# Kernel optimization log

Measured on AMD Instinct MI355X. Metric: run time of the kernel, lower is better.

The kernel has to match this reference:

```python
import jax, jax.numpy as jnp
import numpy as np

NUM_EXPERTS = 4
TOPK = 1
TEMPERATURE = 1.0
NORM_TOPK_PROB = True
N_CLS = 1
N_REL = 4


def setup_inputs() -> dict:
    key = jax.random.key(0)
    ks = jax.random.split(key, 7)
    B, N_total, D, r, E = 64, 1029, 768, 64, NUM_EXPERTS
    x = jax.random.normal(ks[0], (B, N_total, D), dtype=jnp.float32)
    # parameters (torch Linear convention: weight [out, in])
    Wd = jax.random.normal(ks[1], (r, D), dtype=jnp.float32) * (1.0 / np.sqrt(D))
    Wg = jax.random.normal(ks[2], (E, r), dtype=jnp.float32) * (1.0 / np.sqrt(r))
    We = jax.random.normal(ks[3], (E, r, r), dtype=jnp.float32) * (1.0 / np.sqrt(r))
    be = jax.random.normal(ks[4], (E, r), dtype=jnp.float32) * 0.01
    Wu = jax.random.normal(ks[5], (D, r), dtype=jnp.float32) * (1.0 / np.sqrt(r))
    gamma = jnp.ones((D,), dtype=jnp.float32)  # LayerScale init_values=1.0
    return {"x": x, "Wd": Wd, "Wg": Wg, "We": We, "be": be, "Wu": Wu, "gamma": gamma}


def reference(x, Wd, Wg, We, be, Wu, gamma):
    # proj_down (bias=False) + exact GELU (nn.GELU default)
    h = jax.nn.gelu(jnp.einsum('bnd,rd->bnr', x, Wd), approximate=False)  # [B,Nt,r]
    cls_tok = h[:, :N_CLS, :]
    rel_tok = h[:, N_CLS:N_CLS + N_REL, :]
    t = h[:, N_CLS + N_REL:, :]                                           # [B,N,r]
    B, N, r = t.shape

    # gating: softmax scores, top-k selection
    logits = jnp.einsum('bnr,er->bne', t, Wg) / TEMPERATURE
    scores = jax.nn.softmax(logits, axis=-1)                              # [B,N,E]
    topk_w, topk_idx = jax.lax.top_k(scores, TOPK)                        # [B,N,K]
    if TOPK > 1 and NORM_TOPK_PROB:
        topk_w = topk_w / jnp.sum(topk_w, axis=-1, keepdims=True)

    # experts are tiny Linear(r,r): compute all experts densely, then gather.
    # Same math as per-expert gather/GEMM/scatter-combine in the source.
    expert_all = jnp.einsum('bnr,esr->bnes', t, We) + be                  # [B,N,E,r]
    idx_b = jnp.broadcast_to(topk_idx[..., None], (B, N, TOPK, r))
    sel = jnp.take_along_axis(expert_all, idx_b, axis=2)                  # [B,N,K,r]
    combine = jnp.sum(sel * topk_w[..., None], axis=2)                    # [B,N,r]

    full = jnp.concatenate([cls_tok, rel_tok, t + combine], axis=1)       # [B,Nt,r]
    # proj_up (bias=False) + LayerScale
    return jnp.einsum('bnr,dr->bnd', full, Wu) * gamma
```

## Files before the change

kernel.cpp:

```cpp
#include <hip/hip_runtime.h>
#include <math.h>


#define GELU(v) (0.5f*(v)*(1.0f + erff((v)*0.70710678118654752440f)))

typedef __attribute__((ext_vector_type(8))) short bf16x8;
typedef __attribute__((ext_vector_type(4))) float f32x4;

#define MFMA(a,b,c) __builtin_amdgcn_mfma_f32_16x16x32_bf16((a),(b),(c),0,0,0)

__device__ __forceinline__ unsigned pk_hi(float a, float b) {
  return (__float_as_uint(a) >> 16) | (__float_as_uint(b) & 0xFFFF0000u);
}
__device__ __forceinline__ float f_lo(float a) {
  return a - __uint_as_float(__float_as_uint(a) & 0xFFFF0000u);
}
union U8 { unsigned u[4]; bf16x8 v; uint4 q; };
__device__ __forceinline__ bf16x8 hi8(float4 f0, float4 f1) {
  U8 r; r.u[0]=pk_hi(f0.x,f0.y); r.u[1]=pk_hi(f0.z,f0.w);
        r.u[2]=pk_hi(f1.x,f1.y); r.u[3]=pk_hi(f1.z,f1.w); return r.v;
}
__device__ __forceinline__ bf16x8 lo8(float4 f0, float4 f1) {
  U8 r; r.u[0]=pk_hi(f_lo(f0.x),f_lo(f0.y)); r.u[1]=pk_hi(f_lo(f0.z),f_lo(f0.w));
        r.u[2]=pk_hi(f_lo(f1.x),f_lo(f1.y)); r.u[3]=pk_hi(f_lo(f1.z),f_lo(f1.w)); return r.v;
}

__global__ __launch_bounds__(256) void prep_pack(
    const float* __restrict__ Wd, const float* __restrict__ Wg,
    const float* __restrict__ We, const float* __restrict__ Wu,
    char* __restrict__ wp)
{
  int fid = blockIdx.x*4 + (threadIdx.x >> 6);
  if (fid >= 452) return;
  int lane = threadIdx.x & 63, lg = lane >> 4, lr = lane & 15;
  float v[8];
  int part;
  if (fid < 192) {
    part = fid & 1; int q = fid >> 1;
    int nt = q & 3; q >>= 2; int kc = q & 1, kt = q >> 1;
    int col = nt*16 + lr, k = kt*64 + kc*32 + lg*8;
    const float* p = Wd + (size_t)col*768 + k;
    #pragma unroll
    for (int e = 0; e < 8; ++e) v[e] = p[e];
  } else if (fid < 260) {
    int f = fid - 192; part = f & 1; int q = f >> 1;
    int nt = q % 17, kc = q / 17;
    int col = nt*16 + lr, k = kc*32 + lg*8;
    if (col < 256) {
      const float* p = We + (size_t)col*64 + k;
      #pragma unroll
      for (int e = 0; e < 8; ++e) v[e] = p[e];
    } else if (col < 260) {
      const float* p = Wg + (size_t)(col-256)*64 + k;
      #pragma unroll
      for (int e = 0; e < 8; ++e) v[e] = p[e];
    } else {
      #pragma unroll
      for (int e = 0; e < 8; ++e) v[e] = 0.f;
    }
  } else {
    int f = fid - 260; part = f & 1; int q = f >> 1;
    int kc = q & 1, nt = q >> 1;
    int col = nt*16 + lr, k = kc*32 + lg*8;
    const float* p = Wu + (size_t)col*64 + k;
    #pragma unroll
    for (int e = 0; e < 8; ++e) v[e] = p[e];
  }
  U8 r;
  if (part == 0) {
    r.u[0]=pk_hi(v[0],v[1]); r.u[1]=pk_hi(v[2],v[3]);
    r.u[2]=pk_hi(v[4],v[5]); r.u[3]=pk_hi(v[6],v[7]);
  } else {
    r.u[0]=pk_hi(f_lo(v[0]),f_lo(v[1])); r.u[1]=pk_hi(f_lo(v[2]),f_lo(v[3]));
    r.u[2]=pk_hi(f_lo(v[4]),f_lo(v[5])); r.u[3]=pk_hi(f_lo(v[6]),f_lo(v[7]));
  }
  *(uint4*)(wp + (size_t)fid*1024 + lane*16) = r.q;
}

__global__ __launch_bounds__(256) void fused(
    const float* __restrict__ x, const float* __restrict__ be,
    const float* __restrict__ gamma, const char* __restrict__ wp,
    float* __restrict__ out)
{
  __shared__ float sF[4][16][68];
  const int tid = threadIdx.x, bm = blockIdx.x;
  const int wv = tid >> 6, l = tid & 63, lg = l >> 4, lr = l & 15;
  const char* wpL = wp + l*16;

  const float* xrow = x + (size_t)(bm*64 + wv*16 + lr)*768;
  f32x4 t4[4];
  #pragma unroll
  for (int nt = 0; nt < 4; ++nt)
    #pragma unroll
    for (int r = 0; r < 4; ++r) t4[nt][r] = 0.f;

  for (int kt = 0; kt < 12; ++kt) {
    #pragma unroll
    for (int kc = 0; kc < 2; ++kc) {
      const float* xp = xrow + kt*64 + kc*32 + lg*8;
      float4 f0 = *(const float4*)xp, f1 = *(const float4*)(xp + 4);
      bf16x8 ah = hi8(f0, f1), al = lo8(f0, f1);
      const char* bp = wpL + (size_t)((kt*2 + kc)*8)*1024;
      #pragma unroll
      for (int nt = 0; nt < 4; ++nt) {
        bf16x8 bh = *(const bf16x8*)(bp + (nt*2+0)*1024);
        bf16x8 bl = *(const bf16x8*)(bp + (nt*2+1)*1024);
        t4[nt] = MFMA(ah, bh, t4[nt]);
        t4[nt] = MFMA(ah, bl, t4[nt]);
        t4[nt] = MFMA(al, bh, t4[nt]);
      }
    }
  }
  #pragma unroll
  for (int nt = 0; nt < 4; ++nt)
    #pragma unroll
    for (int r = 0; r < 4; ++r) {
      float g = GELU(t4[nt][r]);
      t4[nt][r] = g;
      sF[wv][lg*4 + r][nt*16 + lr] = g;
    }

  bf16x8 pah[2], pal[2];
  #pragma unroll
  for (int kc = 0; kc < 2; ++kc) {
    const float* ap = &sF[wv][lr][kc*32 + lg*8];
    float4 a0 = *(const float4*)ap, a1 = *(const float4*)(ap + 4);
    pah[kc] = hi8(a0, a1); pal[kc] = lo8(a0, a1);
  }
  f32x4 lac;
  #pragma unroll
  for (int r = 0; r < 4; ++r) lac[r] = 0.f;
  #pragma unroll
  for (int kc = 0; kc < 2; ++kc) {
    const char* bp = wpL + (size_t)(192 + (kc*17 + 16)*2)*1024;
    bf16x8 bh = *(const bf16x8*)(bp);
    bf16x8 bl = *(const bf16x8*)(bp + 1024);
    lac = MFMA(pah[kc], bh, lac);
    lac = MFMA(pah[kc], bl, lac);
    lac = MFMA(pal[kc], bh, lac);
  }
  const int tokbase = bm*64 + wv*16 + lg*4;
  float w_[4]; int ei_[4];
  #pragma unroll
  for (int r = 0; r < 4; ++r) {
    float lt = lac[r];
    int base = l & 48;
    float l0 = __shfl(lt, base+0), l1 = __shfl(lt, base+1);
    float l2 = __shfl(lt, base+2), l3 = __shfl(lt, base+3);
    int ei = 0; float lm = l0;
    if (l1 > lm) { lm = l1; ei = 1; }
    if (l2 > lm) { lm = l2; ei = 2; }
    if (l3 > lm) { lm = l3; ei = 3; }
    float s = expf(l0-lm) + expf(l1-lm) + expf(l2-lm) + expf(l3-lm);
    float w = 1.0f / s;
    int pos = (tokbase + r) % 1029;
    if (pos < 5) w = 0.0f;
    w_[r] = w; ei_[r] = ei;
  }
  f32x4 sel[4];
  #pragma unroll
  for (int j = 0; j < 4; ++j)
    #pragma unroll
    for (int r = 0; r < 4; ++r) sel[j][r] = 0.f;
  #pragma unroll
  for (int e = 0; e < 4; ++e) {
    f32x4 de[4];
    #pragma unroll
    for (int j = 0; j < 4; ++j)
      #pragma unroll
      for (int r = 0; r < 4; ++r) de[j][r] = 0.f;
    #pragma unroll
    for (int kc = 0; kc < 2; ++kc) {
      const char* bp = wpL + (size_t)(192 + (kc*17 + e*4)*2)*1024;
      #pragma unroll
      for (int j = 0; j < 4; ++j) {
        bf16x8 bh = *(const bf16x8*)(bp + (j*2+0)*1024);
        bf16x8 bl = *(const bf16x8*)(bp + (j*2+1)*1024);
        de[j] = MFMA(pah[kc], bh, de[j]);
        de[j] = MFMA(pah[kc], bl, de[j]);
        de[j] = MFMA(pal[kc], bh, de[j]);
      }
    }
    #pragma unroll
    for (int j = 0; j < 4; ++j)
      #pragma unroll
      for (int r = 0; r < 4; ++r)
        sel[j][r] = (ei_[r] == e) ? de[j][r] : sel[j][r];
  }
  #pragma unroll
  for (int r = 0; r < 4; ++r) {
    #pragma unroll
    for (int j = 0; j < 4; ++j) {
      int col = j*16 + lr;
      float full = t4[j][r] + w_[r] * (sel[j][r] + be[ei_[r]*64 + col]);
      sF[wv][lg*4 + r][col] = full;
    }
  }

  bf16x8 a3h[2], a3l[2];
  #pragma unroll
  for (int kc = 0; kc < 2; ++kc) {
    const float* ap = &sF[wv][lr][kc*32 + lg*8];
    float4 a0 = *(const float4*)ap, a1 = *(const float4*)(ap + 4);
    a3h[kc] = hi8(a0, a1); a3l[kc] = lo8(a0, a1);
  }
  #pragma unroll 4
  for (int nt = 0; nt < 48; ++nt) {
    const char* bp = wpL + (size_t)(260 + nt*4)*1024;
    f32x4 o;
    #pragma unroll
    for (int r = 0; r < 4; ++r) o[r] = 0.f;
    bf16x8 b0h = *(const bf16x8*)(bp);
    bf16x8 b0l = *(const bf16x8*)(bp + 1024);
    bf16x8 b1h = *(const bf16x8*)(bp + 2048);
    bf16x8 b1l = *(const bf16x8*)(bp + 3072);
    o = MFMA(a3h[0], b0h, o);
    o = MFMA(a3h[0], b0l, o);
    o = MFMA(a3l[0], b0h, o);
    o = MFMA(a3h[1], b1h, o);
    o = MFMA(a3h[1], b1l, o);
    o = MFMA(a3l[1], b1h, o);
    int col = nt*16 + lr;
    float g = gamma[col];
    #pragma unroll
    for (int r = 0; r < 4; ++r)
      out[(size_t)(tokbase + r)*768 + col] = o[r] * g;
  }
}

extern "C" void kernel_launch(void* const* d_in, const int* in_sizes, int n_in,
                              void* d_out, int out_size, void* d_ws, size_t ws_size,
                              hipStream_t stream) {
  const float* x     = (const float*)d_in[0];
  const float* Wd    = (const float*)d_in[1];
  const float* Wg    = (const float*)d_in[2];
  const float* We    = (const float*)d_in[3];
  const float* be    = (const float*)d_in[4];
  const float* Wu    = (const float*)d_in[5];
  const float* gamma = (const float*)d_in[6];
  float* out = (float*)d_out;
  char* wp   = (char*)d_ws;

  prep_pack<<<113, 256, 0, stream>>>(Wd, Wg, We, Wu, wp);
  fused<<<1029, 256, 0, stream>>>(x, be, gamma, (const char*)wp, out);
}
```

Measured before the change: 442.0 us.

## Stage packed weights through LDS with double-buffered async global-to-LDS copies

```diff
diff --git a/kernel.cpp b/kernel.cpp
--- a/kernel.cpp
+++ b/kernel.cpp
@@ -23,6 +23,16 @@
 __device__ __forceinline__ bf16x8 lo8(float4 f0, float4 f1) {
   U8 r; r.u[0]=pk_hi(f_lo(f0.x),f_lo(f0.y)); r.u[1]=pk_hi(f_lo(f0.z),f_lo(f0.w));
         r.u[2]=pk_hi(f_lo(f1.x),f_lo(f1.y)); r.u[3]=pk_hi(f_lo(f1.z),f_lo(f1.w)); return r.v;
+}
+
+__device__ __forceinline__ void cp16(const char* g, char* d, int lane) {
+#if __has_builtin(__builtin_amdgcn_global_load_lds)
+  __builtin_amdgcn_global_load_lds(
+      (const __attribute__((address_space(1))) unsigned int*)g,
+      (__attribute__((address_space(3))) unsigned int*)d, 16, 0, 0);
+#else
+  *(uint4*)(d + lane*16) = *(const uint4*)g;
+#endif
 }
 
 __global__ __launch_bounds__(256) void prep_pack(
@@ -31,86 +41,104 @@
     char* __restrict__ wp)
 {
   int fid = blockIdx.x*4 + (threadIdx.x >> 6);
-  if (fid >= 452) return;
-  int lane = threadIdx.x & 63, lg = lane >> 4, lr = lane & 15;
+  if (fid >= 456) return;
+  int l = threadIdx.x & 63, lg = l >> 4, lr = l & 15;
   float v[8];
-  int part;
+  int part = 0;
   if (fid < 192) {
-    part = fid & 1; int q = fid >> 1;
-    int nt = q & 3; q >>= 2; int kc = q & 1, kt = q >> 1;
-    int col = nt*16 + lr, k = kt*64 + kc*32 + lg*8;
-    const float* p = Wd + (size_t)col*768 + k;
+    int c = fid >> 3, s = fid & 7;
+    int kt = c >> 1, kc = c & 1, nt = s >> 1; part = s & 1;
+    const float* p = Wd + (size_t)(nt*16 + lr)*768 + kt*64 + kc*32 + lg*8;
     #pragma unroll
     for (int e = 0; e < 8; ++e) v[e] = p[e];
-  } else if (fid < 260) {
-    int f = fid - 192; part = f & 1; int q = f >> 1;
-    int nt = q % 17, kc = q / 17;
-    int col = nt*16 + lr, k = kc*32 + lg*8;
-    if (col < 256) {
-      const float* p = We + (size_t)col*64 + k;
+  } else if (fid < 264) {
+    int f = fid - 192, ch = f >> 3, s = f & 7;
+    if (ch == 0) {
+      part = s & 1;
+      int kc = (s >> 1) & 1;
+      if (s < 4 && lr < 4) {
+        const float* p = Wg + lr*64 + kc*32 + lg*8;
+        #pragma unroll
+        for (int e = 0; e < 8; ++e) v[e] = p[e];
+      } else {
+        #pragma unroll
+        for (int e = 0; e < 8; ++e) v[e] = 0.f;
+      }
+    } else {
+      int e_ = (ch - 1) >> 1, kc = (ch - 1) & 1, j = s >> 1; part = s & 1;
+      const float* p = We + (size_t)(e_*64 + j*16 + lr)*64 + kc*32 + lg*8;
       #pragma unroll
       for (int e = 0; e < 8; ++e) v[e] = p[e];
-    } else if (col < 260) {
-      const float* p = Wg + (size_t)(col-256)*64 + k;
-      #pragma unroll
-      for (int e = 0; e < 8; ++e) v[e] = p[e];
-    } else {
-      #pragma unroll
-      for (int e = 0; e < 8; ++e) v[e] = 0.f;
     }
   } else {
-    int f = fid - 260; part = f & 1; int q = f >> 1;
-    int kc = q & 1, nt = q >> 1;
-    int col = nt*16 + lr, k = kc*32 + lg*8;
-    const float* p = Wu + (size_t)col*64 + k;
+    int f = fid - 264;
+    int nt = f >> 2, kc = (f >> 1) & 1; part = f & 1;
+    const float* p = Wu + (size_t)(nt*16 + lr)*64 + kc*32 + lg*8;
     #pragma unroll
     for (int e = 0; e < 8; ++e) v[e] = p[e];
   }
-  U8 r;
+  U8 rr;
   if (part == 0) {
-    r.u[0]=pk_hi(v[0],v[1]); r.u[1]=pk_hi(v[2],v[3]);
-    r.u[2]=pk_hi(v[4],v[5]); r.u[3]=pk_hi(v[6],v[7]);
+    rr.u[0]=pk_hi(v[0],v[1]); rr.u[1]=pk_hi(v[2],v[3]);
+    rr.u[2]=pk_hi(v[4],v[5]); rr.u[3]=pk_hi(v[6],v[7]);
   } else {
-    r.u[0]=pk_hi(f_lo(v[0]),f_lo(v[1])); r.u[1]=pk_hi(f_lo(v[2]),f_lo(v[3]));
-    r.u[2]=pk_hi(f_lo(v[4]),f_lo(v[5])); r.u[3]=pk_hi(f_lo(v[6]),f_lo(v[7]));
-  }
-  *(uint4*)(wp + (size_t)fid*1024 + lane*16) = r.q;
-}
-
-__global__ __launch_bounds__(256) void fused(
+    rr.u[0]=pk_hi(f_lo(v[0]),f_lo(v[1])); rr.u[1]=pk_hi(f_lo(v[2]),f_lo(v[3]));
+    rr.u[2]=pk_hi(f_lo(v[4]),f_lo(v[5])); rr.u[3]=pk_hi(f_lo(v[6]),f_lo(v[7]));
+  }
+  *(uint4*)(wp + (size_t)fid*1024 + (size_t)l*16) = rr.q;
+}
+
+__global__ __launch_bounds__(256, 4) void fused(
     const float* __restrict__ x, const float* __restrict__ be,
     const float* __restrict__ gamma, const char* __restrict__ wp,
     float* __restrict__ out)
 {
   __shared__ float sF[4][16][68];
+  __shared__ char stage[2][8192];
   const int tid = threadIdx.x, bm = blockIdx.x;
   const int wv = tid >> 6, l = tid & 63, lg = l >> 4, lr = l & 15;
-  const char* wpL = wp + l*16;
-
-  const float* xrow = x + (size_t)(bm*64 + wv*16 + lr)*768;
+  const int tokbase = bm*64 + wv*16 + lg*4;
+
+#define STAGE(chunk, buf) do { \
+    const char* _g = wp + (size_t)(chunk)*8192 + (size_t)(wv*2)*1024 + (size_t)l*16; \
+    char* _d = &stage[buf][wv*2048]; \
+    cp16(_g, _d, l); \
+    cp16(_g + 1024, _d + 1024, l); \
+  } while (0)
+
+  const float* xrow = x + (size_t)(bm*64 + wv*16 + lr)*768 + lg*8;
   f32x4 t4[4];
   #pragma unroll
   for (int nt = 0; nt < 4; ++nt)
     #pragma unroll
     for (int r = 0; r < 4; ++r) t4[nt][r] = 0.f;
 
-  for (int kt = 0; kt < 12; ++kt) {
-    #pragma unroll
-    for (int kc = 0; kc < 2; ++kc) {
-      const float* xp = xrow + kt*64 + kc*32 + lg*8;
-      float4 f0 = *(const float4*)xp, f1 = *(const float4*)(xp + 4);
-      bf16x8 ah = hi8(f0, f1), al = lo8(f0, f1);
-      const char* bp = wpL + (size_t)((kt*2 + kc)*8)*1024;
-      #pragma unroll
-      for (int nt = 0; nt < 4; ++nt) {
-        bf16x8 bh = *(const bf16x8*)(bp + (nt*2+0)*1024);
-        bf16x8 bl = *(const bf16x8*)(bp + (nt*2+1)*1024);
-        t4[nt] = MFMA(ah, bh, t4[nt]);
-        t4[nt] = MFMA(ah, bl, t4[nt]);
-        t4[nt] = MFMA(al, bh, t4[nt]);
-      }
-    }
-  }
+  float4 xa = *(const float4*)xrow, xb = *(const float4*)(xrow + 4);
+  STAGE(0, 0);
+  __syncthreads();
+  for (int c = 0; c < 24; ++c) {
+    float4 xa2 = xa, xb2 = xb;
+    if (c < 23) {
+      STAGE(c + 1, (c + 1) & 1);
+      const float* xp = xrow + (c + 1)*32;
+      xa2 = *(const float4*)xp; xb2 = *(const float4*)(xp + 4);
+    }
+    bf16x8 ah = hi8(xa, xb), al = lo8(xa, xb);
+    const char* bp = &stage[c & 1][l*16];
+    #pragma unroll
+    for (int nt = 0; nt < 4; ++nt) {
+      bf16x8 bh = *(const bf16x8*)(bp + (size_t)(nt*2)*1024);
+      bf16x8 bl = *(const bf16x8*)(bp + (size_t)(nt*2 + 1)*1024);
+      t4[nt] = MFMA(ah, bh, t4[nt]);
+      t4[nt] = MFMA(ah, bl, t4[nt]);
+      t4[nt] = MFMA(al, bh, t4[nt]);
+    }
+    __syncthreads();
+    xa = xa2; xb = xb2;
+  }
+
+  STAGE(24, 0);
+  STAGE(25, 1);
   #pragma unroll
   for (int nt = 0; nt < 4; ++nt)
     #pragma unroll
@@ -119,7 +147,6 @@
       t4[nt][r] = g;
       sF[wv][lg*4 + r][nt*16 + lr] = g;
     }
-
   bf16x8 pah[2], pal[2];
   #pragma unroll
   for (int kc = 0; kc < 2; ++kc) {
@@ -127,76 +154,81 @@
     float4 a0 = *(const float4*)ap, a1 = *(const float4*)(ap + 4);
     pah[kc] = hi8(a0, a1); pal[kc] = lo8(a0, a1);
   }
+  __syncthreads();
+
   f32x4 lac;
   #pragma unroll
   for (int r = 0; r < 4; ++r) lac[r] = 0.f;
-  #pragma unroll
-  for (int kc = 0; kc < 2; ++kc) {
-    const char* bp = wpL + (size_t)(192 + (kc*17 + 16)*2)*1024;
-    bf16x8 bh = *(const bf16x8*)(bp);
-    bf16x8 bl = *(const bf16x8*)(bp + 1024);
-    lac = MFMA(pah[kc], bh, lac);
-    lac = MFMA(pah[kc], bl, lac);
-    lac = MFMA(pal[kc], bh, lac);
-  }
-  const int tokbase = bm*64 + wv*16 + lg*4;
+  {
+    const char* bp = &stage[0][l*16];
+    bf16x8 b0h = *(const bf16x8*)(bp);
+    bf16x8 b0l = *(const bf16x8*)(bp + 1024);
+    bf16x8 b1h = *(const bf16x8*)(bp + 2048);
+    bf16x8 b1l = *(const bf16x8*)(bp + 3072);
+    lac = MFMA(pah[0], b0h, lac); lac = MFMA(pah[0], b0l, lac); lac = MFMA(pal[0], b0h, lac);
+    lac = MFMA(pah[1], b1h, lac); lac = MFMA(pah[1], b1l, lac); lac = MFMA(pal[1], b1h, lac);
+  }
   float w_[4]; int ei_[4];
   #pragma unroll
   for (int r = 0; r < 4; ++r) {
     float lt = lac[r];
     int base = l & 48;
-    float l0 = __shfl(lt, base+0), l1 = __shfl(lt, base+1);
-    float l2 = __shfl(lt, base+2), l3 = __shfl(lt, base+3);
+    float l0 = __shfl(lt, base + 0), l1 = __shfl(lt, base + 1);
+    float l2 = __shfl(lt, base + 2), l3 = __shfl(lt, base + 3);
     int ei = 0; float lm = l0;
     if (l1 > lm) { lm = l1; ei = 1; }
     if (l2 > lm) { lm = l2; ei = 2; }
     if (l3 > lm) { lm = l3; ei = 3; }
-    float s = expf(l0-lm) + expf(l1-lm) + expf(l2-lm) + expf(l3-lm);
+    float s = expf(l0 - lm) + expf(l1 - lm) + expf(l2 - lm) + expf(l3 - lm);
     float w = 1.0f / s;
     int pos = (tokbase + r) % 1029;
     if (pos < 5) w = 0.0f;
     w_[r] = w; ei_[r] = ei;
   }
-  f32x4 sel[4];
+  __syncthreads();
+  STAGE(26, 0);
+
+  f32x4 de[4], sel[4];
   #pragma unroll
   for (int j = 0; j < 4; ++j)
     #pragma unroll
-    for (int r = 0; r < 4; ++r) sel[j][r] = 0.f;
-  #pragma unroll
-  for (int e = 0; e < 4; ++e) {
-    f32x4 de[4];
-    #pragma unroll
-    for (int j = 0; j < 4; ++j)
-      #pragma unroll
-      for (int r = 0; r < 4; ++r) de[j][r] = 0.f;
-    #pragma unroll
-    for (int kc = 0; kc < 2; ++kc) {
-      const char* bp = wpL + (size_t)(192 + (kc*17 + e*4)*2)*1024;
-      #pragma unroll
-      for (int j = 0; j < 4; ++j) {
-        bf16x8 bh = *(const bf16x8*)(bp + (j*2+0)*1024);
-        bf16x8 bl = *(const bf16x8*)(bp + (j*2+1)*1024);
-        de[j] = MFMA(pah[kc], bh, de[j]);
-        de[j] = MFMA(pah[kc], bl, de[j]);
-        de[j] = MFMA(pal[kc], bh, de[j]);
-      }
-    }
-    #pragma unroll
-    for (int j = 0; j < 4; ++j)
-      #pragma unroll
-      for (int r = 0; r < 4; ++r)
-        sel[j][r] = (ei_[r] == e) ? de[j][r] : sel[j][r];
-  }
-  #pragma unroll
-  for (int r = 0; r < 4; ++r) {
+    for (int r = 0; r < 4; ++r) { de[j][r] = 0.f; sel[j][r] = 0.f; }
+
+  #pragma unroll
+  for (int s = 1; s <= 8; ++s) {
+    const int e_ = (s - 1) >> 1, kc = (s - 1) & 1, cb = s & 1;
+    const char* bp = &stage[cb][l*16];
+    #pragma unroll
+    for (int j = 0; j < 4; ++j) {
+      bf16x8 bh = *(const bf16x8*)(bp + (size_t)(j*2)*1024);
+      bf16x8 bl = *(const bf16x8*)(bp + (size_t)(j*2 + 1)*1024);
+      de[j] = MFMA(pah[kc], bh, de[j]);
+      de[j] = MFMA(pah[kc], bl, de[j]);
+      de[j] = MFMA(pal[kc], bh, de[j]);
+    }
+    if (kc == 1) {
+      #pragma unroll
+      for (int j = 0; j < 4; ++j)
+        #pragma unroll
+        for (int r = 0; r < 4; ++r) {
+          sel[j][r] = (ei_[r] == e_) ? de[j][r] : sel[j][r];
+          de[j][r] = 0.f;
+        }
+    }
+    __syncthreads();
+    if (s <= 6) STAGE(26 + s, cb);
+  }
+
+  STAGE(33, 1);
+  STAGE(34, 0);
+  #pragma unroll
+  for (int r = 0; r < 4; ++r)
     #pragma unroll
     for (int j = 0; j < 4; ++j) {
       int col = j*16 + lr;
       float full = t4[j][r] + w_[r] * (sel[j][r] + be[ei_[r]*64 + col]);
       sF[wv][lg*4 + r][col] = full;
     }
-  }
-
   bf16x8 a3h[2], a3l[2];
   #pragma unroll
   for (int kc = 0; kc < 2; ++kc) {
@@ -204,28 +236,33 @@
     float4 a0 = *(const float4*)ap, a1 = *(const float4*)(ap + 4);
     a3h[kc] = hi8(a0, a1); a3l[kc] = lo8(a0, a1);
   }
-  #pragma unroll 4
-  for (int nt = 0; nt < 48; ++nt) {
-    const char* bp = wpL + (size_t)(260 + nt*4)*1024;
-    f32x4 o;
-    #pragma unroll
-    for (int r = 0; r < 4; ++r) o[r] = 0.f;
-    bf16x8 b0h = *(const bf16x8*)(bp);
-    bf16x8 b0l = *(const bf16x8*)(bp + 1024);
-    bf16x8 b1h = *(const bf16x8*)(bp + 2048);
-    bf16x8 b1l = *(const bf16x8*)(bp + 3072);
-    o = MFMA(a3h[0], b0h, o);
-    o = MFMA(a3h[0], b0l, o);
-    o = MFMA(a3l[0], b0h, o);
-    o = MFMA(a3h[1], b1h, o);
-    o = MFMA(a3h[1], b1l, o);
-    o = MFMA(a3l[1], b1h, o);
-    int col = nt*16 + lr;
-    float g = gamma[col];
-    #pragma unroll
-    for (int r = 0; r < 4; ++r)
-      out[(size_t)(tokbase + r)*768 + col] = o[r] * g;
-  }
+  __syncthreads();
+
+  for (int c = 0; c < 24; ++c) {
+    const int cb = (c + 1) & 1;
+    const char* bpc = &stage[cb][l*16];
+    #pragma unroll
+    for (int u = 0; u < 2; ++u) {
+      const char* bp = bpc + u*4096;
+      bf16x8 b0h = *(const bf16x8*)(bp);
+      bf16x8 b0l = *(const bf16x8*)(bp + 1024);
+      bf16x8 b1h = *(const bf16x8*)(bp + 2048);
+      bf16x8 b1l = *(const bf16x8*)(bp + 3072);
+      f32x4 o;
+      #pragma unroll
+      for (int r = 0; r < 4; ++r) o[r] = 0.f;
+      o = MFMA(a3h[0], b0h, o); o = MFMA(a3h[0], b0l, o); o = MFMA(a3l[0], b0h, o);
+      o = MFMA(a3h[1], b1h, o); o = MFMA(a3h[1], b1l, o); o = MFMA(a3l[1], b1h, o);
+      const int col = (c*2 + u)*16 + lr;
+      const float gv = gamma[col];
+      #pragma unroll
+      for (int r = 0; r < 4; ++r)
+        out[(size_t)(tokbase + r)*768 + col] = o[r] * gv;
+    }
+    __syncthreads();
+    if (c + 2 < 24) STAGE(35 + c, cb);
+  }
+#undef STAGE
 }
 
 extern "C" void kernel_launch(void* const* d_in, const int* in_sizes, int n_in,
@@ -241,6 +278,6 @@
   float* out = (float*)d_out;
   char* wp   = (char*)d_ws;
 
-  prep_pack<<<113, 256, 0, stream>>>(Wd, Wg, We, Wu, wp);
+  prep_pack<<<114, 256, 0, stream>>>(Wd, Wg, We, Wu, wp);
   fused<<<1029, 256, 0, stream>>>(x, be, gamma, (const char*)wp, out);
 }
```

Measured after the change: 428.7 us. 3.0% less time.
